# Kernel optimization log

Hardware: AMD Instinct MI355X
Metric: run time of the kernel (lower is better)

The kernel has to match this reference:

```python
import jax, jax.numpy as jnp
import numpy as np

DIM = 96; D_STATE = 16; D_CONV = 4; EXPAND = 2
D_INNER = EXPAND * DIM          # 192
DT_RANK = (DIM + 15) // 16      # 6
B, H, W = 4, 64, 64


def setup_inputs() -> dict:
    key = jax.random.key(0)
    ks = jax.random.split(key, 10)
    r = lambda k, shp, s=0.02: jax.random.normal(k, shp, jnp.float32) * s
    return {
        "x": jax.random.normal(ks[0], (B, DIM, H, W), jnp.float32),
        "norm_g": jnp.ones((DIM,), jnp.float32),
        "norm_b": jnp.zeros((DIM,), jnp.float32),
        "gate_w1": r(ks[1], (DIM // 4, DIM)),
        "gate_b1": jnp.zeros((DIM // 4,), jnp.float32),
        "gate_w2": r(ks[2], (4, DIM // 4)),
        "gate_b2": jnp.zeros((4,), jnp.float32),
        "in_proj_w": r(ks[3], (2 * D_INNER, DIM)),
        "conv_w": r(ks[4], (D_INNER, 1, D_CONV), 0.1),
        "conv_b": jnp.zeros((D_INNER,), jnp.float32),
        "x_proj_w": r(ks[5], (DT_RANK + 2 * D_STATE, D_INNER)),
        "dt_proj_w": r(ks[6], (D_INNER, DT_RANK), 0.1),
        "dt_proj_b": jnp.full((D_INNER,), -2.0, jnp.float32) + r(ks[7], (D_INNER,), 0.1),
        "A_log": jnp.log(jnp.broadcast_to(jnp.arange(1, D_STATE + 1, dtype=jnp.float32), (D_INNER, D_STATE))),
        "D": jnp.ones((D_INNER,), jnp.float32),
        "out_proj_w": r(ks[8], (DIM, D_INNER)),
    }


def _mamba(u, in_proj_w, conv_w, conv_b, x_proj_w, dt_proj_w, dt_proj_b, A_log, Dp, out_proj_w):
    # u: (N, L, DIM)
    N, L, _ = u.shape
    xz = jnp.einsum('nld,ed->nle', u, in_proj_w)            # (N, L, 2*d_inner)
    xs, z = jnp.split(xz, 2, axis=-1)
    # depthwise causal conv1d along L
    xc = jax.lax.conv_general_dilated(xs.transpose(0, 2, 1), conv_w, (1,),
                                      [(D_CONV - 1, 0)], feature_group_count=D_INNER)
    xc = jax.nn.silu(xc + conv_b[None, :, None]).transpose(0, 2, 1)   # (N, L, d_inner)
    x_dbl = jnp.einsum('nld,ed->nle', xc, x_proj_w)
    dt, Bm, Cm = jnp.split(x_dbl, [DT_RANK, DT_RANK + D_STATE], axis=-1)
    delta = jax.nn.softplus(jnp.einsum('nlr,dr->nld', dt, dt_proj_w) + dt_proj_b)  # (N, L, d_inner)
    A = -jnp.exp(A_log)                                     # (d_inner, d_state)

    def step(h, inp):
        u_t, d_t, B_t, C_t = inp                            # (N,di) (N,di) (N,ds) (N,ds)
        dA = jnp.exp(d_t[:, :, None] * A)                   # (N, di, ds)
        h = dA * h + (d_t * u_t)[:, :, None] * B_t[:, None, :]
        y_t = jnp.einsum('nds,ns->nd', h, C_t)
        return h, y_t

    h0 = jnp.zeros((N, D_INNER, D_STATE), xc.dtype)
    xsw = (xc.transpose(1, 0, 2), delta.transpose(1, 0, 2),
           Bm.transpose(1, 0, 2), Cm.transpose(1, 0, 2))
    _, ys = jax.lax.scan(step, h0, xsw)                     # ys: (L, N, di)
    y = ys.transpose(1, 0, 2) + xc * Dp
    y = y * jax.nn.silu(z)
    return jnp.einsum('nld,od->nlo', y, out_proj_w)         # (N, L, DIM)


def reference(x, norm_g, norm_b, gate_w1, gate_b1, gate_w2, gate_b2,
              in_proj_w, conv_w, conv_b, x_proj_w, dt_proj_w, dt_proj_b,
              A_log, D, out_proj_w):
    Bb, C, Hh, Ww = x.shape
    L = Hh * Ww
    xp = x.transpose(0, 2, 3, 1)                            # (B, H, W, C)
    mu = xp.mean(-1, keepdims=True)
    var = xp.var(-1, keepdims=True)
    xn = (xp - mu) * jax.lax.rsqrt(var + 1e-5) * norm_g + norm_b
    gate = jax.nn.softmax(jnp.tanh(xn @ gate_w1.T + gate_b1) @ gate_w2.T + gate_b2, axis=-1)  # (B,H,W,4)
    xcln = xn.transpose(0, 3, 1, 2)                         # (B, C, H, W)
    x_hw = xcln.reshape(Bb, C, L).transpose(0, 2, 1)        # row-major scan
    x_wh = xcln.transpose(0, 1, 3, 2).reshape(Bb, C, L).transpose(0, 2, 1)  # col-major scan
    seqs = jnp.concatenate([x_hw, x_wh, x_hw[:, ::-1], x_wh[:, ::-1]], axis=0)  # (4B, L, C)
    outs = _mamba(seqs, in_proj_w, conv_w, conv_b, x_proj_w, dt_proj_w,
                  dt_proj_b, A_log, D, out_proj_w)
    o1, o2, o3, o4 = jnp.split(outs, 4, axis=0)
    y1 = o1.transpose(0, 2, 1).reshape(Bb, C, Hh, Ww)
    y2 = o2.transpose(0, 2, 1).reshape(Bb, C, Ww, Hh).transpose(0, 1, 3, 2)
    y3 = o3[:, ::-1].transpose(0, 2, 1).reshape(Bb, C, Hh, Ww)
    y4 = o4[:, ::-1].transpose(0, 2, 1).reshape(Bb, C, Ww, Hh).transpose(0, 1, 3, 2)
    ys = jnp.stack([y1, y2, y3, y4], axis=-1).transpose(0, 2, 3, 1, 4)  # (B,H,W,C,4)
    yf = (ys * gate[:, :, :, None, :]).sum(-1)              # (B, H, W, C)
    return yf.transpose(0, 3, 1, 2)
```

## Files before the change

kernel.cpp:

```cpp
#include <hip/hip_runtime.h>
#include <math.h>

#define CH   96
#define HW   4096
#define DI   192
#define DS   16
#define XD   38
#define CL   32
#define NCHK 128

typedef short bf16x8 __attribute__((ext_vector_type(8)));
typedef float f32x4 __attribute__((ext_vector_type(4)));

__device__ __forceinline__ int pmap(int dir, int l) {
  if (dir == 0) return l;
  if (dir == 1) return ((l & 63) << 6) | (l >> 6);
  if (dir == 2) return 4095 - l;
  int m = 4095 - l;
  return ((m & 63) << 6) | (m >> 6);
}

__device__ __forceinline__ float sigm(float x) { return 1.f / (1.f + __expf(-x)); }
__device__ __forceinline__ float siluf(float x) { return x * sigm(x); }
__device__ __forceinline__ unsigned short f2bf(float v) {
  unsigned u = __float_as_uint(v);
  u += 0x7fffu + ((u >> 16) & 1u);
  return (unsigned short)(u >> 16);
}
__device__ __forceinline__ float bf2f(unsigned short v) {
  return __uint_as_float((unsigned)v << 16);
}

__global__ __launch_bounds__(256) void k_ln_gate(
    const float* __restrict__ x, const float* __restrict__ ng, const float* __restrict__ nb,
    const float* __restrict__ gw1, const float* __restrict__ gb1,
    const float* __restrict__ gw2, const float* __restrict__ gb2,
    unsigned short* __restrict__ xn, float* __restrict__ gate) {
  __shared__ float tile[CH * 65];
  __shared__ float ps[256], pq[256], mu_s[64], rs_s[64];
  __shared__ float hid[24 * 64];
  int t = threadIdx.x;
  int b = blockIdx.x >> 6;
  int p0 = (blockIdx.x & 63) << 6;
  #pragma unroll
  for (int i = 0; i < 24; i++) {
    int f = i * 256 + t;
    int c = f >> 6, p = f & 63;
    tile[c * 65 + p] = x[(size_t)(b * CH + c) * HW + p0 + p];
  }
  __syncthreads();
  int p = t & 63, g = t >> 6;
  float s = 0.f, q = 0.f;
  #pragma unroll
  for (int i = 0; i < 24; i++) {
    float v = tile[(g * 24 + i) * 65 + p];
    s += v; q += v * v;
  }
  ps[g * 64 + p] = s; pq[g * 64 + p] = q;
  __syncthreads();
  if (t < 64) {
    float ss = ps[t] + ps[64 + t] + ps[128 + t] + ps[192 + t];
    float qq = pq[t] + pq[64 + t] + pq[128 + t] + pq[192 + t];
    float mu = ss * (1.f / 96.f);
    float var = qq * (1.f / 96.f) - mu * mu;
    mu_s[t] = mu;
    rs_s[t] = rsqrtf(var + 1e-5f);
  }
  __syncthreads();
  float mu = mu_s[p], rs = rs_s[p];
  #pragma unroll
  for (int i = 0; i < 24; i++) {
    int c = g * 24 + i;
    float v = (tile[c * 65 + p] - mu) * rs * ng[c] + nb[c];
    tile[c * 65 + p] = v;
  }
  __syncthreads();
  #pragma unroll
  for (int i = 0; i < 24; i++) {
    int f = i * 256 + t;
    int c = f % 96, pp = f / 96;
    xn[(size_t)(b * HW + p0 + pp) * CH + c] = f2bf(tile[c * 65 + pp]);
  }
  {
    int j0 = g * 6;
    #pragma unroll
    for (int jj = 0; jj < 6; jj++) {
      int j = j0 + jj;
      float acc = gb1[j];
      for (int c = 0; c < 96; c++) acc = fmaf(gw1[j * 96 + c], tile[c * 65 + p], acc);
      hid[j * 64 + p] = tanhf(acc);
    }
  }
  __syncthreads();
  if (t < 64) {
    float lg[4];
    #pragma unroll
    for (int k = 0; k < 4; k++) {
      float acc = gb2[k];
      #pragma unroll
      for (int j = 0; j < 24; j++) acc = fmaf(gw2[k * 24 + j], hid[j * 64 + t], acc);
      lg[k] = acc;
    }
    float m = fmaxf(fmaxf(lg[0], lg[1]), fmaxf(lg[2], lg[3]));
    float e0 = __expf(lg[0] - m), e1 = __expf(lg[1] - m);
    float e2 = __expf(lg[2] - m), e3 = __expf(lg[3] - m);
    float inv = 1.f / (e0 + e1 + e2 + e3);
    size_t gi = (size_t)(b * HW + p0 + t) * 4;
    gate[gi] = e0 * inv; gate[gi + 1] = e1 * inv;
    gate[gi + 2] = e2 * inv; gate[gi + 3] = e3 * inv;
  }
}

__global__ __launch_bounds__(256) void k_inproj(
    const unsigned short* __restrict__ xn, const float* __restrict__ W,
    unsigned short* __restrict__ xz) {
  __shared__ unsigned short Wl[96 * 104];
  int t = threadIdx.x;
  int ns = blockIdx.y * 96;
  for (int f = t; f < 96 * 96; f += 256) {
    int r = f / 96, c = f - r * 96;
    Wl[r * 104 + c] = f2bf(W[(ns + r) * 96 + c]);
  }
  __syncthreads();
  int lane = t & 63, wv = t >> 6;
  int quad = lane >> 4, lm = lane & 15;
  int m0 = (blockIdx.x << 6) + (wv << 4);
  const unsigned short* arow = xn + (size_t)(m0 + lm) * 96 + quad * 8;
  bf16x8 afr[3];
  #pragma unroll
  for (int s = 0; s < 3; s++) afr[s] = *(const bf16x8*)(arow + s * 32);
  f32x4 acc[6];
  #pragma unroll
  for (int j = 0; j < 6; j++) acc[j] = (f32x4){0.f, 0.f, 0.f, 0.f};
  #pragma unroll
  for (int j = 0; j < 6; j++) {
    const unsigned short* wrow = &Wl[(j * 16 + lm) * 104 + quad * 8];
    #pragma unroll
    for (int s = 0; s < 3; s++) {
      bf16x8 bfr = *(const bf16x8*)(wrow + s * 32);
      acc[j] = __builtin_amdgcn_mfma_f32_16x16x32_bf16(afr[s], bfr, acc[j], 0, 0, 0);
    }
  }
  #pragma unroll
  for (int j = 0; j < 6; j++)
    #pragma unroll
    for (int reg = 0; reg < 4; reg++)
      xz[(size_t)(m0 + quad * 4 + reg) * 384 + ns + j * 16 + lm] = f2bf(acc[j][reg]);
}

__global__ __launch_bounds__(256) void k_xproj(
    const unsigned short* __restrict__ xc, const float* __restrict__ W,
    float* __restrict__ xdbl) {
  __shared__ unsigned short Wl[48 * 200];
  int t = threadIdx.x;
  for (int f = t; f < 48 * 192; f += 256) {
    int r = f / 192, c = f - r * 192;
    Wl[r * 200 + c] = (r < XD) ? f2bf(W[r * 192 + c]) : 0;
  }
  __syncthreads();
  int lane = t & 63, wv = t >> 6;
  int quad = lane >> 4, lm = lane & 15;
  int m0 = (blockIdx.x << 6) + (wv << 4);
  const unsigned short* arow = xc + (size_t)(m0 + lm) * DI + quad * 8;
  bf16x8 afr[6];
  #pragma unroll
  for (int s = 0; s < 6; s++) afr[s] = *(const bf16x8*)(arow + s * 32);
  f32x4 acc[3];
  #pragma unroll
  for (int j = 0; j < 3; j++) acc[j] = (f32x4){0.f, 0.f, 0.f, 0.f};
  #pragma unroll
  for (int j = 0; j < 3; j++) {
    const unsigned short* wrow = &Wl[(j * 16 + lm) * 200 + quad * 8];
    #pragma unroll
    for (int s = 0; s < 6; s++) {
      bf16x8 bfr = *(const bf16x8*)(wrow + s * 32);
      acc[j] = __builtin_amdgcn_mfma_f32_16x16x32_bf16(afr[s], bfr, acc[j], 0, 0, 0);
    }
  }
  #pragma unroll
  for (int j = 0; j < 3; j++) {
    int col = j * 16 + lm;
    if (col < XD)
      #pragma unroll
      for (int reg = 0; reg < 4; reg++)
        xdbl[(size_t)(m0 + quad * 4 + reg) * XD + col] = acc[j][reg];
  }
}

__global__ __launch_bounds__(192) void k_conv(
    const unsigned short* __restrict__ xz, const float* __restrict__ cw,
    const float* __restrict__ cb, unsigned short* __restrict__ xc) {
  int t = threadIdx.x;
  int n = blockIdx.x >> 7;
  int c = blockIdx.x & 127;
  int l0 = c << 5;
  int dir = n >> 2, b = n & 3;
  int d = t;
  float w0 = cw[d * 4], w1 = cw[d * 4 + 1], w2 = cw[d * 4 + 2], w3 = cw[d * 4 + 3];
  float bias = cb[d];
  float xm3 = (l0 >= 3) ? bf2f(xz[(size_t)(b * HW + pmap(dir, l0 - 3)) * 384 + d]) : 0.f;
  float xm2 = (l0 >= 2) ? bf2f(xz[(size_t)(b * HW + pmap(dir, l0 - 2)) * 384 + d]) : 0.f;
  float xm1 = (l0 >= 1) ? bf2f(xz[(size_t)(b * HW + pmap(dir, l0 - 1)) * 384 + d]) : 0.f;
  #pragma unroll 4
  for (int l = 0; l < 32; l++) {
    float xcur = bf2f(xz[(size_t)(b * HW + pmap(dir, l0 + l)) * 384 + d]);
    float acc = fmaf(w0, xm3, bias);
    acc = fmaf(w1, xm2, acc);
    acc = fmaf(w2, xm1, acc);
    acc = fmaf(w3, xcur, acc);
    xc[(size_t)(n * HW + l0 + l) * DI + d] = f2bf(siluf(acc));
    xm3 = xm2; xm2 = xm1; xm1 = xcur;
  }
}

__global__ __launch_bounds__(64) void k_scan1(
    const unsigned short* __restrict__ xc, const float* __restrict__ xdbl,
    const float* __restrict__ dtw, const float* __restrict__ dtb,
    float* __restrict__ Pbuf, float* __restrict__ hpart) {
  int bx = blockIdx.x;
  int dg = bx % 3;
  int nc = bx / 3;
  int n = nc >> 7;
  int c = nc & 127;
  int l0 = c << 5;
  int d = dg * 64 + threadIdx.x;
  float w0 = dtw[d * 6 + 0], w1 = dtw[d * 6 + 1], w2 = dtw[d * 6 + 2],
        w3 = dtw[d * 6 + 3], w4 = dtw[d * 6 + 4], w5 = dtw[d * 6 + 5];
  float b0 = dtb[d];
  float h[DS];
  #pragma unroll
  for (int s = 0; s < DS; s++) h[s] = 0.f;
  float P = 1.f;
  #pragma unroll 8
  for (int l = 0; l < CL; l++) {
    size_t row = (size_t)(n * HW + l0 + l);
    const float* rp = xdbl + row * XD;
    float acc = b0;
    acc = fmaf(rp[0], w0, acc); acc = fmaf(rp[1], w1, acc);
    acc = fmaf(rp[2], w2, acc); acc = fmaf(rp[3], w3, acc);
    acc = fmaf(rp[4], w4, acc); acc = fmaf(rp[5], w5, acc);
    float ex = __expf(acc);
    float e1 = __builtin_amdgcn_rcpf(1.f + ex);
    float dlt = (acc > 15.f) ? acc : -__logf(e1);
    float u = bf2f(xc[row * DI + d]);
    P *= e1;
    float du = dlt * u;
    float e2 = e1 * e1, e4 = e2 * e2, e3 = e1 * e2;
    float q0 = e1, q1 = e2, q2 = e3, q3 = e4;
    h[0]  = fmaf(q0, h[0],  du * rp[6]);  h[1]  = fmaf(q1, h[1],  du * rp[7]);
    h[2]  = fmaf(q2, h[2],  du * rp[8]);  h[3]  = fmaf(q3, h[3],  du * rp[9]);
    q0 *= e4; q1 *= e4; q2 *= e4; q3 *= e4;
    h[4]  = fmaf(q0, h[4],  du * rp[10]); h[5]  = fmaf(q1, h[5],  du * rp[11]);
    h[6]  = fmaf(q2, h[6],  du * rp[12]); h[7]  = fmaf(q3, h[7],  du * rp[13]);
    q0 *= e4; q1 *= e4; q2 *= e4; q3 *= e4;
    h[8]  = fmaf(q0, h[8],  du * rp[14]); h[9]  = fmaf(q1, h[9],  du * rp[15]);
    h[10] = fmaf(q2, h[10], du * rp[16]); h[11] = fmaf(q3, h[11], du * rp[17]);
    q0 *= e4; q1 *= e4; q2 *= e4; q3 *= e4;
    h[12] = fmaf(q0, h[12], du * rp[18]); h[13] = fmaf(q1, h[13], du * rp[19]);
    h[14] = fmaf(q2, h[14], du * rp[20]); h[15] = fmaf(q3, h[15], du * rp[21]);
  }
  size_t bi = ((size_t)n * DI + d) * NCHK + c;
  Pbuf[bi] = P;
  float4* hp = (float4*)&hpart[bi * 16];
  hp[0] = make_float4(h[0], h[1], h[2], h[3]);
  hp[1] = make_float4(h[4], h[5], h[6], h[7]);
  hp[2] = make_float4(h[8], h[9], h[10], h[11]);
  hp[3] = make_float4(h[12], h[13], h[14], h[15]);
}

__global__ __launch_bounds__(256) void k_scan2(
    const float* __restrict__ Pbuf, const float* __restrict__ hpart,
    float* __restrict__ hstart) {
  int g = blockIdx.x * 256 + threadIdx.x;
  int s = g & 15;
  int nd = g >> 4;
  float hs = 0.f;
  size_t base = (size_t)nd * NCHK;
  int e = s + 1;
  for (int c0 = 0; c0 < NCHK; c0 += 8) {
    float part[8], Pp[8];
    #pragma unroll
    for (int i = 0; i < 8; i++) {
      part[i] = hpart[(base + c0 + i) * 16 + s];
      Pp[i]   = Pbuf[base + c0 + i];
    }
    #pragma unroll
    for (int i = 0; i < 8; i++) {
      hstart[(base + c0 + i) * 16 + s] = hs;
      float pw = 1.f, bse = Pp[i];
      int ee = e;
      while (ee) { if (ee & 1) pw *= bse; bse *= bse; ee >>= 1; }
      hs = fmaf(pw, hs, part[i]);
    }
  }
}

__global__ __launch_bounds__(64) void k_scan3(
    const unsigned short* __restrict__ xc, const float* __restrict__ xdbl,
    const float* __restrict__ dtw, const float* __restrict__ dtb,
    const float* __restrict__ hstart, const unsigned short* __restrict__ xz,
    const float* __restrict__ Dp, const float* __restrict__ gate,
    float* __restrict__ yc) {
  int bx = blockIdx.x;
  int dg = bx % 3;
  int nc = bx / 3;
  int n = nc >> 7;
  int cch = nc & 127;
  int l0 = cch << 5;
  int dir = n >> 2, b = n & 3;
  int d = dg * 64 + threadIdx.x;
  float w0 = dtw[d * 6 + 0], w1 = dtw[d * 6 + 1], w2 = dtw[d * 6 + 2],
        w3 = dtw[d * 6 + 3], w4 = dtw[d * 6 + 4], w5 = dtw[d * 6 + 5];
  float b0 = dtb[d];
  size_t bi = ((size_t)n * DI + d) * NCHK + cch;
  const float4* hp = (const float4*)&hstart[bi * 16];
  float4 h0 = hp[0], h1 = hp[1], h2 = hp[2], h3 = hp[3];
  float h[DS] = {h0.x, h0.y, h0.z, h0.w, h1.x, h1.y, h1.z, h1.w,
                 h2.x, h2.y, h2.z, h2.w, h3.x, h3.y, h3.z, h3.w};
  float Dd = Dp[d];
  #pragma unroll 8
  for (int l = 0; l < CL; l++) {
    size_t row = (size_t)(n * HW + l0 + l);
    const float* rp = xdbl + row * XD;
    float acc = b0;
    acc = fmaf(rp[0], w0, acc); acc = fmaf(rp[1], w1, acc);
    acc = fmaf(rp[2], w2, acc); acc = fmaf(rp[3], w3, acc);
    acc = fmaf(rp[4], w4, acc); acc = fmaf(rp[5], w5, acc);
    float ex = __expf(acc);
    float e1 = __builtin_amdgcn_rcpf(1.f + ex);
    float dlt = (acc > 15.f) ? acc : -__logf(e1);
    float u = bf2f(xc[row * DI + d]);
    float du = dlt * u;
    float e2 = e1 * e1, e4 = e2 * e2, e3 = e1 * e2;
    float q0 = e1, q1 = e2, q2 = e3, q3 = e4;
    float y0 = 0.f, y1 = 0.f, y2 = 0.f, y3 = 0.f;
    h[0]  = fmaf(q0, h[0],  du * rp[6]);  h[1]  = fmaf(q1, h[1],  du * rp[7]);
    h[2]  = fmaf(q2, h[2],  du * rp[8]);  h[3]  = fmaf(q3, h[3],  du * rp[9]);
    y0 = fmaf(h[0], rp[22], y0); y1 = fmaf(h[1], rp[23], y1);
    y2 = fmaf(h[2], rp[24], y2); y3 = fmaf(h[3], rp[25], y3);
    q0 *= e4; q1 *= e4; q2 *= e4; q3 *= e4;
    h[4]  = fmaf(q0, h[4],  du * rp[10]); h[5]  = fmaf(q1, h[5],  du * rp[11]);
    h[6]  = fmaf(q2, h[6],  du * rp[12]); h[7]  = fmaf(q3, h[7],  du * rp[13]);
    y0 = fmaf(h[4], rp[26], y0); y1 = fmaf(h[5], rp[27], y1);
    y2 = fmaf(h[6], rp[28], y2); y3 = fmaf(h[7], rp[29], y3);
    q0 *= e4; q1 *= e4; q2 *= e4; q3 *= e4;
    h[8]  = fmaf(q0, h[8],  du * rp[14]); h[9]  = fmaf(q1, h[9],  du * rp[15]);
    h[10] = fmaf(q2, h[10], du * rp[16]); h[11] = fmaf(q3, h[11], du * rp[17]);
    y0 = fmaf(h[8], rp[30], y0); y1 = fmaf(h[9], rp[31], y1);
    y2 = fmaf(h[10], rp[32], y2); y3 = fmaf(h[11], rp[33], y3);
    q0 *= e4; q1 *= e4; q2 *= e4; q3 *= e4;
    h[12] = fmaf(q0, h[12], du * rp[18]); h[13] = fmaf(q1, h[13], du * rp[19]);
    h[14] = fmaf(q2, h[14], du * rp[20]); h[15] = fmaf(q3, h[15], du * rp[21]);
    y0 = fmaf(h[12], rp[34], y0); y1 = fmaf(h[13], rp[35], y1);
    y2 = fmaf(h[14], rp[36], y2); y3 = fmaf(h[15], rp[37], y3);
    float yv = (y0 + y1) + (y2 + y3);
    int p = pmap(dir, l0 + l);
    float z = bf2f(xz[(size_t)(b * HW + p) * 384 + 192 + d]);
    float g = gate[((size_t)(b * HW) + p) * 4 + dir];
    atomicAdd(&yc[(size_t)(b * HW + p) * DI + d],
              g * ((yv + u * Dd) * siluf(z)));
  }
}

__global__ __launch_bounds__(256) void k_outproj(
    const float* __restrict__ yc, const float* __restrict__ W,
    float* __restrict__ out) {
  __shared__ unsigned short Wl[96 * 200];
  __shared__ float Ct[64 * 97];
  int t = threadIdx.x;
  for (int f = t; f < 96 * 192; f += 256) {
    int r = f / 192, c = f - r * 192;
    Wl[r * 200 + c] = f2bf(W[f]);
  }
  __syncthreads();
  int lane = t & 63, wv = t >> 6;
  int quad = lane >> 4, lm = lane & 15;
  int m0 = (blockIdx.x << 6) + (wv << 4);
  const float* arow = yc + (size_t)(m0 + lm) * DI + quad * 8;
  bf16x8 afr[6];
  #pragma unroll
  for (int s = 0; s < 6; s++) {
    float4 a0 = *(const float4*)(arow + s * 32);
    float4 a1 = *(const float4*)(arow + s * 32 + 4);
    bf16x8 v;
    v[0] = (short)f2bf(a0.x); v[1] = (short)f2bf(a0.y);
    v[2] = (short)f2bf(a0.z); v[3] = (short)f2bf(a0.w);
    v[4] = (short)f2bf(a1.x); v[5] = (short)f2bf(a1.y);
    v[6] = (short)f2bf(a1.z); v[7] = (short)f2bf(a1.w);
    afr[s] = v;
  }
  f32x4 acc[6];
  #pragma unroll
  for (int j = 0; j < 6; j++) acc[j] = (f32x4){0.f, 0.f, 0.f, 0.f};
  #pragma unroll
  for (int j = 0; j < 6; j++) {
    const unsigned short* wrow = &Wl[(j * 16 + lm) * 200 + quad * 8];
    #pragma unroll
    for (int s = 0; s < 6; s++) {
      bf16x8 bfr = *(const bf16x8*)(wrow + s * 32);
      acc[j] = __builtin_amdgcn_mfma_f32_16x16x32_bf16(afr[s], bfr, acc[j], 0, 0, 0);
    }
  }
  #pragma unroll
  for (int j = 0; j < 6; j++)
    #pragma unroll
    for (int reg = 0; reg < 4; reg++)
      Ct[((wv << 4) + (quad << 2) + reg) * 97 + j * 16 + lm] = acc[j][reg];
  __syncthreads();
  int blk = blockIdx.x << 6;
  int b = blk >> 12, P0 = blk & 4095;
  int p = t & 63;
  #pragma unroll
  for (int i = 0; i < 24; i++) {
    int cc = i * 4 + (t >> 6);
    out[(size_t)(b * CH + cc) * HW + P0 + p] = Ct[p * 97 + cc];
  }
}

extern "C" void kernel_launch(void* const* d_in, const int* in_sizes, int n_in,
                              void* d_out, int out_size, void* d_ws, size_t ws_size,
                              hipStream_t stream) {
  const float* x   = (const float*)d_in[0];
  const float* ng  = (const float*)d_in[1];
  const float* nb  = (const float*)d_in[2];
  const float* gw1 = (const float*)d_in[3];
  const float* gb1 = (const float*)d_in[4];
  const float* gw2 = (const float*)d_in[5];
  const float* gb2 = (const float*)d_in[6];
  const float* ipw = (const float*)d_in[7];
  const float* cw  = (const float*)d_in[8];
  const float* cb  = (const float*)d_in[9];
  const float* xpw = (const float*)d_in[10];
  const float* dtw = (const float*)d_in[11];
  const float* dtb = (const float*)d_in[12];
  const float* Dp  = (const float*)d_in[14];
  const float* opw = (const float*)d_in[15];
  float* out = (float*)d_out;

  float* ws = (float*)d_ws;
  float* xn     = ws;
  float* gate   = xn     + (size_t)786432;
  float* xz     = gate   + (size_t)65536;
  float* xc     = xz     + (size_t)3145728;
  float* xdbl   = xc     + (size_t)6291456;
  float* yc     = xdbl   + (size_t)2490368;
  float* Pbuf   = yc     + (size_t)3145728;
  float* hpart  = Pbuf   + (size_t)16 * 192 * NCHK;
  float* hstart = hpart  + (size_t)16 * 192 * NCHK * 16;
  unsigned short* xnh   = (unsigned short*)xn;
  unsigned short* xzh   = (unsigned short*)xz;
  unsigned short* xch   = (unsigned short*)xc;

  k_ln_gate<<<256, 256, 0, stream>>>(x, ng, nb, gw1, gb1, gw2, gb2, xnh, gate);
  k_inproj<<<dim3(256, 4), 256, 0, stream>>>(xnh, ipw, xzh);
  k_conv<<<2048, 192, 0, stream>>>(xzh, cw, cb, xch);
  k_xproj<<<1024, 256, 0, stream>>>(xch, xpw, xdbl);
  k_scan1<<<6144, 64, 0, stream>>>(xch, xdbl, dtw, dtb, Pbuf, hpart);
  hipMemsetAsync(yc, 0, (size_t)16384 * 192 * sizeof(float), stream);
  k_scan2<<<192, 256, 0, stream>>>(Pbuf, hpart, hstart);
  k_scan3<<<6144, 64, 0, stream>>>(xch, xdbl, dtw, dtb, hstart, xzh, Dp, gate, yc);
  k_outproj<<<256, 256, 0, stream>>>(yc, opw, out);
}
```

Baseline: 261.9 us.

## Compute local scan outputs in first pass and correct with carried state later

```diff
diff --git a/kernel.cpp b/kernel.cpp
--- a/kernel.cpp
+++ b/kernel.cpp
@@ -29,6 +29,10 @@
 }
 __device__ __forceinline__ float bf2f(unsigned short v) {
   return __uint_as_float((unsigned)v << 16);
+}
+__device__ __forceinline__ unsigned pack_py(float P, float yp) {
+  unsigned short ph = __builtin_bit_cast(unsigned short, (_Float16)P);
+  return ((unsigned)f2bf(yp) << 16) | (unsigned)ph;
 }
 
 __global__ __launch_bounds__(256) void k_ln_gate(
@@ -216,7 +220,8 @@
 __global__ __launch_bounds__(64) void k_scan1(
     const unsigned short* __restrict__ xc, const float* __restrict__ xdbl,
     const float* __restrict__ dtw, const float* __restrict__ dtb,
-    float* __restrict__ Pbuf, float* __restrict__ hpart) {
+    const float* __restrict__ Dp,
+    float* __restrict__ Pbuf, float* __restrict__ hpart, unsigned* __restrict__ yP) {
   int bx = blockIdx.x;
   int dg = bx % 3;
   int nc = bx / 3;
@@ -227,6 +232,7 @@
   float w0 = dtw[d * 6 + 0], w1 = dtw[d * 6 + 1], w2 = dtw[d * 6 + 2],
         w3 = dtw[d * 6 + 3], w4 = dtw[d * 6 + 4], w5 = dtw[d * 6 + 5];
   float b0 = dtb[d];
+  float Dd = Dp[d];
   float h[DS];
   #pragma unroll
   for (int s = 0; s < DS; s++) h[s] = 0.f;
@@ -244,92 +250,6 @@
     float dlt = (acc > 15.f) ? acc : -__logf(e1);
     float u = bf2f(xc[row * DI + d]);
     P *= e1;
-    float du = dlt * u;
-    float e2 = e1 * e1, e4 = e2 * e2, e3 = e1 * e2;
-    float q0 = e1, q1 = e2, q2 = e3, q3 = e4;
-    h[0]  = fmaf(q0, h[0],  du * rp[6]);  h[1]  = fmaf(q1, h[1],  du * rp[7]);
-    h[2]  = fmaf(q2, h[2],  du * rp[8]);  h[3]  = fmaf(q3, h[3],  du * rp[9]);
-    q0 *= e4; q1 *= e4; q2 *= e4; q3 *= e4;
-    h[4]  = fmaf(q0, h[4],  du * rp[10]); h[5]  = fmaf(q1, h[5],  du * rp[11]);
-    h[6]  = fmaf(q2, h[6],  du * rp[12]); h[7]  = fmaf(q3, h[7],  du * rp[13]);
-    q0 *= e4; q1 *= e4; q2 *= e4; q3 *= e4;
-    h[8]  = fmaf(q0, h[8],  du * rp[14]); h[9]  = fmaf(q1, h[9],  du * rp[15]);
-    h[10] = fmaf(q2, h[10], du * rp[16]); h[11] = fmaf(q3, h[11], du * rp[17]);
-    q0 *= e4; q1 *= e4; q2 *= e4; q3 *= e4;
-    h[12] = fmaf(q0, h[12], du * rp[18]); h[13] = fmaf(q1, h[13], du * rp[19]);
-    h[14] = fmaf(q2, h[14], du * rp[20]); h[15] = fmaf(q3, h[15], du * rp[21]);
-  }
-  size_t bi = ((size_t)n * DI + d) * NCHK + c;
-  Pbuf[bi] = P;
-  float4* hp = (float4*)&hpart[bi * 16];
-  hp[0] = make_float4(h[0], h[1], h[2], h[3]);
-  hp[1] = make_float4(h[4], h[5], h[6], h[7]);
-  hp[2] = make_float4(h[8], h[9], h[10], h[11]);
-  hp[3] = make_float4(h[12], h[13], h[14], h[15]);
-}
-
-__global__ __launch_bounds__(256) void k_scan2(
-    const float* __restrict__ Pbuf, const float* __restrict__ hpart,
-    float* __restrict__ hstart) {
-  int g = blockIdx.x * 256 + threadIdx.x;
-  int s = g & 15;
-  int nd = g >> 4;
-  float hs = 0.f;
-  size_t base = (size_t)nd * NCHK;
-  int e = s + 1;
-  for (int c0 = 0; c0 < NCHK; c0 += 8) {
-    float part[8], Pp[8];
-    #pragma unroll
-    for (int i = 0; i < 8; i++) {
-      part[i] = hpart[(base + c0 + i) * 16 + s];
-      Pp[i]   = Pbuf[base + c0 + i];
-    }
-    #pragma unroll
-    for (int i = 0; i < 8; i++) {
-      hstart[(base + c0 + i) * 16 + s] = hs;
-      float pw = 1.f, bse = Pp[i];
-      int ee = e;
-      while (ee) { if (ee & 1) pw *= bse; bse *= bse; ee >>= 1; }
-      hs = fmaf(pw, hs, part[i]);
-    }
-  }
-}
-
-__global__ __launch_bounds__(64) void k_scan3(
-    const unsigned short* __restrict__ xc, const float* __restrict__ xdbl,
-    const float* __restrict__ dtw, const float* __restrict__ dtb,
-    const float* __restrict__ hstart, const unsigned short* __restrict__ xz,
-    const float* __restrict__ Dp, const float* __restrict__ gate,
-    float* __restrict__ yc) {
-  int bx = blockIdx.x;
-  int dg = bx % 3;
-  int nc = bx / 3;
-  int n = nc >> 7;
-  int cch = nc & 127;
-  int l0 = cch << 5;
-  int dir = n >> 2, b = n & 3;
-  int d = dg * 64 + threadIdx.x;
-  float w0 = dtw[d * 6 + 0], w1 = dtw[d * 6 + 1], w2 = dtw[d * 6 + 2],
-        w3 = dtw[d * 6 + 3], w4 = dtw[d * 6 + 4], w5 = dtw[d * 6 + 5];
-  float b0 = dtb[d];
-  size_t bi = ((size_t)n * DI + d) * NCHK + cch;
-  const float4* hp = (const float4*)&hstart[bi * 16];
-  float4 h0 = hp[0], h1 = hp[1], h2 = hp[2], h3 = hp[3];
-  float h[DS] = {h0.x, h0.y, h0.z, h0.w, h1.x, h1.y, h1.z, h1.w,
-                 h2.x, h2.y, h2.z, h2.w, h3.x, h3.y, h3.z, h3.w};
-  float Dd = Dp[d];
-  #pragma unroll 8
-  for (int l = 0; l < CL; l++) {
-    size_t row = (size_t)(n * HW + l0 + l);
-    const float* rp = xdbl + row * XD;
-    float acc = b0;
-    acc = fmaf(rp[0], w0, acc); acc = fmaf(rp[1], w1, acc);
-    acc = fmaf(rp[2], w2, acc); acc = fmaf(rp[3], w3, acc);
-    acc = fmaf(rp[4], w4, acc); acc = fmaf(rp[5], w5, acc);
-    float ex = __expf(acc);
-    float e1 = __builtin_amdgcn_rcpf(1.f + ex);
-    float dlt = (acc > 15.f) ? acc : -__logf(e1);
-    float u = bf2f(xc[row * DI + d]);
     float du = dlt * u;
     float e2 = e1 * e1, e4 = e2 * e2, e3 = e1 * e2;
     float q0 = e1, q1 = e2, q2 = e3, q3 = e4;
@@ -353,12 +273,88 @@
     h[14] = fmaf(q2, h[14], du * rp[20]); h[15] = fmaf(q3, h[15], du * rp[21]);
     y0 = fmaf(h[12], rp[34], y0); y1 = fmaf(h[13], rp[35], y1);
     y2 = fmaf(h[14], rp[36], y2); y3 = fmaf(h[15], rp[37], y3);
-    float yv = (y0 + y1) + (y2 + y3);
+    float yv = ((y0 + y1) + (y2 + y3)) + u * Dd;
+    yP[row * DI + d] = pack_py(P, yv);
+  }
+  size_t bi = ((size_t)n * DI + d) * NCHK + c;
+  Pbuf[bi] = P;
+  float4* hp = (float4*)&hpart[bi * 16];
+  hp[0] = make_float4(h[0], h[1], h[2], h[3]);
+  hp[1] = make_float4(h[4], h[5], h[6], h[7]);
+  hp[2] = make_float4(h[8], h[9], h[10], h[11]);
+  hp[3] = make_float4(h[12], h[13], h[14], h[15]);
+}
+
+__global__ __launch_bounds__(256) void k_scan2(
+    const float* __restrict__ Pbuf, const float* __restrict__ hpart,
+    float* __restrict__ hstart) {
+  int g = blockIdx.x * 256 + threadIdx.x;
+  int s = g & 15;
+  int nd = g >> 4;
+  float hs = 0.f;
+  size_t base = (size_t)nd * NCHK;
+  int e = s + 1;
+  for (int c0 = 0; c0 < NCHK; c0 += 8) {
+    float part[8], Pp[8];
+    #pragma unroll
+    for (int i = 0; i < 8; i++) {
+      part[i] = hpart[(base + c0 + i) * 16 + s];
+      Pp[i]   = Pbuf[base + c0 + i];
+    }
+    #pragma unroll
+    for (int i = 0; i < 8; i++) {
+      hstart[(base + c0 + i) * 16 + s] = hs;
+      float pw = 1.f, bse = Pp[i];
+      int ee = e;
+      while (ee) { if (ee & 1) pw *= bse; bse *= bse; ee >>= 1; }
+      hs = fmaf(pw, hs, part[i]);
+    }
+  }
+}
+
+__global__ __launch_bounds__(64) void k_scan3(
+    const unsigned* __restrict__ yP, const float* __restrict__ xdbl,
+    const float* __restrict__ hstart, const unsigned short* __restrict__ xz,
+    const float* __restrict__ gate, float* __restrict__ yc) {
+  int bx = blockIdx.x;
+  int dg = bx % 3;
+  int nc = bx / 3;
+  int n = nc >> 7;
+  int cch = nc & 127;
+  int l0 = cch << 5;
+  int dir = n >> 2, b = n & 3;
+  int d = dg * 64 + threadIdx.x;
+  size_t bi = ((size_t)n * DI + d) * NCHK + cch;
+  const float4* hp = (const float4*)&hstart[bi * 16];
+  float4 h0 = hp[0], h1 = hp[1], h2 = hp[2], h3 = hp[3];
+  float h[DS] = {h0.x, h0.y, h0.z, h0.w, h1.x, h1.y, h1.z, h1.w,
+                 h2.x, h2.y, h2.z, h2.w, h3.x, h3.y, h3.z, h3.w};
+  #pragma unroll 8
+  for (int l = 0; l < CL; l++) {
+    size_t row = (size_t)(n * HW + l0 + l);
+    const float* rp = xdbl + row * XD;
+    unsigned pk = yP[row * DI + d];
+    float P  = (float)__builtin_bit_cast(_Float16, (unsigned short)(pk & 0xffffu));
+    float yp = bf2f((unsigned short)(pk >> 16));
+    float P2 = P * P, P4 = P2 * P2, P3 = P * P2;
+    float q0 = P, q1 = P2, q2 = P3, q3 = P4;
+    float y0 = 0.f, y1 = 0.f, y2 = 0.f, y3 = 0.f;
+    y0 = fmaf(h[0] * q0, rp[22], y0);  y1 = fmaf(h[1] * q1, rp[23], y1);
+    y2 = fmaf(h[2] * q2, rp[24], y2);  y3 = fmaf(h[3] * q3, rp[25], y3);
+    q0 *= P4; q1 *= P4; q2 *= P4; q3 *= P4;
+    y0 = fmaf(h[4] * q0, rp[26], y0);  y1 = fmaf(h[5] * q1, rp[27], y1);
+    y2 = fmaf(h[6] * q2, rp[28], y2);  y3 = fmaf(h[7] * q3, rp[29], y3);
+    q0 *= P4; q1 *= P4; q2 *= P4; q3 *= P4;
+    y0 = fmaf(h[8] * q0, rp[30], y0);  y1 = fmaf(h[9] * q1, rp[31], y1);
+    y2 = fmaf(h[10] * q2, rp[32], y2); y3 = fmaf(h[11] * q3, rp[33], y3);
+    q0 *= P4; q1 *= P4; q2 *= P4; q3 *= P4;
+    y0 = fmaf(h[12] * q0, rp[34], y0); y1 = fmaf(h[13] * q1, rp[35], y1);
+    y2 = fmaf(h[14] * q2, rp[36], y2); y3 = fmaf(h[15] * q3, rp[37], y3);
+    float yv = yp + ((y0 + y1) + (y2 + y3));
     int p = pmap(dir, l0 + l);
     float z = bf2f(xz[(size_t)(b * HW + p) * 384 + 192 + d]);
     float g = gate[((size_t)(b * HW) + p) * 4 + dir];
-    atomicAdd(&yc[(size_t)(b * HW + p) * DI + d],
-              g * ((yv + u * Dd) * siluf(z)));
+    atomicAdd(&yc[(size_t)(b * HW + p) * DI + d], g * (yv * siluf(z)));
   }
 }
 
@@ -447,17 +443,19 @@
   float* Pbuf   = yc     + (size_t)3145728;
   float* hpart  = Pbuf   + (size_t)16 * 192 * NCHK;
   float* hstart = hpart  + (size_t)16 * 192 * NCHK * 16;
+  float* yPf    = hstart + (size_t)16 * 192 * NCHK * 16;
   unsigned short* xnh   = (unsigned short*)xn;
   unsigned short* xzh   = (unsigned short*)xz;
   unsigned short* xch   = (unsigned short*)xc;
+  unsigned* yP = (unsigned*)yPf;
 
   k_ln_gate<<<256, 256, 0, stream>>>(x, ng, nb, gw1, gb1, gw2, gb2, xnh, gate);
   k_inproj<<<dim3(256, 4), 256, 0, stream>>>(xnh, ipw, xzh);
   k_conv<<<2048, 192, 0, stream>>>(xzh, cw, cb, xch);
   k_xproj<<<1024, 256, 0, stream>>>(xch, xpw, xdbl);
-  k_scan1<<<6144, 64, 0, stream>>>(xch, xdbl, dtw, dtb, Pbuf, hpart);
+  k_scan1<<<6144, 64, 0, stream>>>(xch, xdbl, dtw, dtb, Dp, Pbuf, hpart, yP);
   hipMemsetAsync(yc, 0, (size_t)16384 * 192 * sizeof(float), stream);
   k_scan2<<<192, 256, 0, stream>>>(Pbuf, hpart, hstart);
-  k_scan3<<<6144, 64, 0, stream>>>(xch, xdbl, dtw, dtb, hstart, xzh, Dp, gate, yc);
+  k_scan3<<<6144, 64, 0, stream>>>(yP, xdbl, hstart, xzh, gate, yc);
   k_outproj<<<256, 256, 0, stream>>>(yc, opw, out);
 }
```

After: 284.6 us. 8.7% more time.

## Pair opposite-direction scan chunks per block to replace atomics with plain stores

Applied to the files above, without the earlier changes.

```diff
diff --git a/kernel.cpp b/kernel.cpp
--- a/kernel.cpp
+++ b/kernel.cpp
@@ -300,71 +300,85 @@
     const float* __restrict__ dtw, const float* __restrict__ dtb,
     const float* __restrict__ hstart, const unsigned short* __restrict__ xz,
     const float* __restrict__ Dp, const float* __restrict__ gate,
-    float* __restrict__ yc) {
+    float* __restrict__ yc_a, float* __restrict__ yc_b) {
+  __shared__ float accs[CL * 64];
   int bx = blockIdx.x;
   int dg = bx % 3;
-  int nc = bx / 3;
-  int n = nc >> 7;
-  int cch = nc & 127;
-  int l0 = cch << 5;
-  int dir = n >> 2, b = n & 3;
-  int d = dg * 64 + threadIdx.x;
+  int rest = bx / 3;
+  int c = rest & 127;
+  int b = (rest >> 7) & 3;
+  int pair = rest >> 9;
+  int t = threadIdx.x;
+  int d = dg * 64 + t;
   float w0 = dtw[d * 6 + 0], w1 = dtw[d * 6 + 1], w2 = dtw[d * 6 + 2],
         w3 = dtw[d * 6 + 3], w4 = dtw[d * 6 + 4], w5 = dtw[d * 6 + 5];
   float b0 = dtb[d];
-  size_t bi = ((size_t)n * DI + d) * NCHK + cch;
-  const float4* hp = (const float4*)&hstart[bi * 16];
-  float4 h0 = hp[0], h1 = hp[1], h2 = hp[2], h3 = hp[3];
-  float h[DS] = {h0.x, h0.y, h0.z, h0.w, h1.x, h1.y, h1.z, h1.w,
-                 h2.x, h2.y, h2.z, h2.w, h3.x, h3.y, h3.z, h3.w};
   float Dd = Dp[d];
-  #pragma unroll 8
-  for (int l = 0; l < CL; l++) {
-    size_t row = (size_t)(n * HW + l0 + l);
-    const float* rp = xdbl + row * XD;
-    float acc = b0;
-    acc = fmaf(rp[0], w0, acc); acc = fmaf(rp[1], w1, acc);
-    acc = fmaf(rp[2], w2, acc); acc = fmaf(rp[3], w3, acc);
-    acc = fmaf(rp[4], w4, acc); acc = fmaf(rp[5], w5, acc);
-    float ex = __expf(acc);
-    float e1 = __builtin_amdgcn_rcpf(1.f + ex);
-    float dlt = (acc > 15.f) ? acc : -__logf(e1);
-    float u = bf2f(xc[row * DI + d]);
-    float du = dlt * u;
-    float e2 = e1 * e1, e4 = e2 * e2, e3 = e1 * e2;
-    float q0 = e1, q1 = e2, q2 = e3, q3 = e4;
-    float y0 = 0.f, y1 = 0.f, y2 = 0.f, y3 = 0.f;
-    h[0]  = fmaf(q0, h[0],  du * rp[6]);  h[1]  = fmaf(q1, h[1],  du * rp[7]);
-    h[2]  = fmaf(q2, h[2],  du * rp[8]);  h[3]  = fmaf(q3, h[3],  du * rp[9]);
-    y0 = fmaf(h[0], rp[22], y0); y1 = fmaf(h[1], rp[23], y1);
-    y2 = fmaf(h[2], rp[24], y2); y3 = fmaf(h[3], rp[25], y3);
-    q0 *= e4; q1 *= e4; q2 *= e4; q3 *= e4;
-    h[4]  = fmaf(q0, h[4],  du * rp[10]); h[5]  = fmaf(q1, h[5],  du * rp[11]);
-    h[6]  = fmaf(q2, h[6],  du * rp[12]); h[7]  = fmaf(q3, h[7],  du * rp[13]);
-    y0 = fmaf(h[4], rp[26], y0); y1 = fmaf(h[5], rp[27], y1);
-    y2 = fmaf(h[6], rp[28], y2); y3 = fmaf(h[7], rp[29], y3);
-    q0 *= e4; q1 *= e4; q2 *= e4; q3 *= e4;
-    h[8]  = fmaf(q0, h[8],  du * rp[14]); h[9]  = fmaf(q1, h[9],  du * rp[15]);
-    h[10] = fmaf(q2, h[10], du * rp[16]); h[11] = fmaf(q3, h[11], du * rp[17]);
-    y0 = fmaf(h[8], rp[30], y0); y1 = fmaf(h[9], rp[31], y1);
-    y2 = fmaf(h[10], rp[32], y2); y3 = fmaf(h[11], rp[33], y3);
-    q0 *= e4; q1 *= e4; q2 *= e4; q3 *= e4;
-    h[12] = fmaf(q0, h[12], du * rp[18]); h[13] = fmaf(q1, h[13], du * rp[19]);
-    h[14] = fmaf(q2, h[14], du * rp[20]); h[15] = fmaf(q3, h[15], du * rp[21]);
-    y0 = fmaf(h[12], rp[34], y0); y1 = fmaf(h[13], rp[35], y1);
-    y2 = fmaf(h[14], rp[36], y2); y3 = fmaf(h[15], rp[37], y3);
-    float yv = (y0 + y1) + (y2 + y3);
-    int p = pmap(dir, l0 + l);
-    float z = bf2f(xz[(size_t)(b * HW + p) * 384 + 192 + d]);
-    float g = gate[((size_t)(b * HW) + p) * 4 + dir];
-    atomicAdd(&yc[(size_t)(b * HW + p) * DI + d],
-              g * ((yv + u * Dd) * siluf(z)));
+  float* ycp = pair ? yc_b : yc_a;
+  #pragma unroll
+  for (int pass = 0; pass < 2; pass++) {
+    int dir = (pair ? 1 : 0) + (pass ? 2 : 0);
+    int cch = pass ? (127 - c) : c;
+    int n = (dir << 2) + b;
+    int l0 = cch << 5;
+    size_t bi = ((size_t)n * DI + d) * NCHK + cch;
+    const float4* hp = (const float4*)&hstart[bi * 16];
+    float4 h0 = hp[0], h1 = hp[1], h2 = hp[2], h3 = hp[3];
+    float h[DS] = {h0.x, h0.y, h0.z, h0.w, h1.x, h1.y, h1.z, h1.w,
+                   h2.x, h2.y, h2.z, h2.w, h3.x, h3.y, h3.z, h3.w};
+    #pragma unroll 4
+    for (int j = 0; j < CL; j++) {
+      size_t row = (size_t)(n * HW + l0 + j);
+      const float* rp = xdbl + row * XD;
+      float acc = b0;
+      acc = fmaf(rp[0], w0, acc); acc = fmaf(rp[1], w1, acc);
+      acc = fmaf(rp[2], w2, acc); acc = fmaf(rp[3], w3, acc);
+      acc = fmaf(rp[4], w4, acc); acc = fmaf(rp[5], w5, acc);
+      float ex = __expf(acc);
+      float e1 = __builtin_amdgcn_rcpf(1.f + ex);
+      float dlt = (acc > 15.f) ? acc : -__logf(e1);
+      float u = bf2f(xc[row * DI + d]);
+      float du = dlt * u;
+      float e2 = e1 * e1, e4 = e2 * e2, e3 = e1 * e2;
+      float q0 = e1, q1 = e2, q2 = e3, q3 = e4;
+      float y0 = 0.f, y1 = 0.f, y2 = 0.f, y3 = 0.f;
+      h[0]  = fmaf(q0, h[0],  du * rp[6]);  h[1]  = fmaf(q1, h[1],  du * rp[7]);
+      h[2]  = fmaf(q2, h[2],  du * rp[8]);  h[3]  = fmaf(q3, h[3],  du * rp[9]);
+      y0 = fmaf(h[0], rp[22], y0); y1 = fmaf(h[1], rp[23], y1);
+      y2 = fmaf(h[2], rp[24], y2); y3 = fmaf(h[3], rp[25], y3);
+      q0 *= e4; q1 *= e4; q2 *= e4; q3 *= e4;
+      h[4]  = fmaf(q0, h[4],  du * rp[10]); h[5]  = fmaf(q1, h[5],  du * rp[11]);
+      h[6]  = fmaf(q2, h[6],  du * rp[12]); h[7]  = fmaf(q3, h[7],  du * rp[13]);
+      y0 = fmaf(h[4], rp[26], y0); y1 = fmaf(h[5], rp[27], y1);
+      y2 = fmaf(h[6], rp[28], y2); y3 = fmaf(h[7], rp[29], y3);
+      q0 *= e4; q1 *= e4; q2 *= e4; q3 *= e4;
+      h[8]  = fmaf(q0, h[8],  du * rp[14]); h[9]  = fmaf(q1, h[9],  du * rp[15]);
+      h[10] = fmaf(q2, h[10], du * rp[16]); h[11] = fmaf(q3, h[11], du * rp[17]);
+      y0 = fmaf(h[8], rp[30], y0); y1 = fmaf(h[9], rp[31], y1);
+      y2 = fmaf(h[10], rp[32], y2); y3 = fmaf(h[11], rp[33], y3);
+      q0 *= e4; q1 *= e4; q2 *= e4; q3 *= e4;
+      h[12] = fmaf(q0, h[12], du * rp[18]); h[13] = fmaf(q1, h[13], du * rp[19]);
+      h[14] = fmaf(q2, h[14], du * rp[20]); h[15] = fmaf(q3, h[15], du * rp[21]);
+      y0 = fmaf(h[12], rp[34], y0); y1 = fmaf(h[13], rp[35], y1);
+      y2 = fmaf(h[14], rp[36], y2); y3 = fmaf(h[15], rp[37], y3);
+      float yv = ((y0 + y1) + (y2 + y3)) + u * Dd;
+      int p = pmap(dir, l0 + j);
+      float z = bf2f(xz[(size_t)(b * HW + p) * 384 + 192 + d]);
+      float g = gate[((size_t)(b * HW) + p) * 4 + dir];
+      float contrib = g * (yv * siluf(z));
+      if (pass == 0) {
+        accs[j * 64 + t] = contrib;
+      } else {
+        int w = 31 - j;
+        ycp[(size_t)(b * HW + p) * DI + d] = accs[w * 64 + t] + contrib;
+      }
+    }
   }
 }
 
 __global__ __launch_bounds__(256) void k_outproj(
-    const float* __restrict__ yc, const float* __restrict__ W,
-    float* __restrict__ out) {
+    const float* __restrict__ yc_a, const float* __restrict__ yc_b,
+    const float* __restrict__ W, float* __restrict__ out) {
   __shared__ unsigned short Wl[96 * 200];
   __shared__ float Ct[64 * 97];
   int t = threadIdx.x;
@@ -376,17 +390,19 @@
   int lane = t & 63, wv = t >> 6;
   int quad = lane >> 4, lm = lane & 15;
   int m0 = (blockIdx.x << 6) + (wv << 4);
-  const float* arow = yc + (size_t)(m0 + lm) * DI + quad * 8;
+  size_t aoff = (size_t)(m0 + lm) * DI + quad * 8;
   bf16x8 afr[6];
   #pragma unroll
   for (int s = 0; s < 6; s++) {
-    float4 a0 = *(const float4*)(arow + s * 32);
-    float4 a1 = *(const float4*)(arow + s * 32 + 4);
+    float4 a0 = *(const float4*)(yc_a + aoff + s * 32);
+    float4 a1 = *(const float4*)(yc_a + aoff + s * 32 + 4);
+    float4 c0 = *(const float4*)(yc_b + aoff + s * 32);
+    float4 c1 = *(const float4*)(yc_b + aoff + s * 32 + 4);
     bf16x8 v;
-    v[0] = (short)f2bf(a0.x); v[1] = (short)f2bf(a0.y);
-    v[2] = (short)f2bf(a0.z); v[3] = (short)f2bf(a0.w);
-    v[4] = (short)f2bf(a1.x); v[5] = (short)f2bf(a1.y);
-    v[6] = (short)f2bf(a1.z); v[7] = (short)f2bf(a1.w);
+    v[0] = (short)f2bf(a0.x + c0.x); v[1] = (short)f2bf(a0.y + c0.y);
+    v[2] = (short)f2bf(a0.z + c0.z); v[3] = (short)f2bf(a0.w + c0.w);
+    v[4] = (short)f2bf(a1.x + c1.x); v[5] = (short)f2bf(a1.y + c1.y);
+    v[6] = (short)f2bf(a1.z + c1.z); v[7] = (short)f2bf(a1.w + c1.w);
     afr[s] = v;
   }
   f32x4 acc[6];
@@ -443,8 +459,9 @@
   float* xz     = gate   + (size_t)65536;
   float* xc     = xz     + (size_t)3145728;
   float* xdbl   = xc     + (size_t)6291456;
-  float* yc     = xdbl   + (size_t)2490368;
-  float* Pbuf   = yc     + (size_t)3145728;
+  float* yc_a   = xdbl   + (size_t)2490368;
+  float* yc_b   = yc_a   + (size_t)3145728;
+  float* Pbuf   = yc_b   + (size_t)3145728;
   float* hpart  = Pbuf   + (size_t)16 * 192 * NCHK;
   float* hstart = hpart  + (size_t)16 * 192 * NCHK * 16;
   unsigned short* xnh   = (unsigned short*)xn;
@@ -456,8 +473,7 @@
   k_conv<<<2048, 192, 0, stream>>>(xzh, cw, cb, xch);
   k_xproj<<<1024, 256, 0, stream>>>(xch, xpw, xdbl);
   k_scan1<<<6144, 64, 0, stream>>>(xch, xdbl, dtw, dtb, Pbuf, hpart);
-  hipMemsetAsync(yc, 0, (size_t)16384 * 192 * sizeof(float), stream);
   k_scan2<<<192, 256, 0, stream>>>(Pbuf, hpart, hstart);
-  k_scan3<<<6144, 64, 0, stream>>>(xch, xdbl, dtw, dtb, hstart, xzh, Dp, gate, yc);
-  k_outproj<<<256, 256, 0, stream>>>(yc, opw, out);
-}
+  k_scan3<<<3072, 64, 0, stream>>>(xch, xdbl, dtw, dtb, hstart, xzh, Dp, gate, yc_a, yc_b);
+  k_outproj<<<256, 256, 0, stream>>>(yc_a, yc_b, opw, out);
+}
```

New measurement: 275.5 us. +5.2%, slower.
